# Kernel optimization log

Measured on AMD Instinct MI355X. Metric: run time of the kernel, lower is better.

The kernel has to match this reference:

```python
import jax, jax.numpy as jnp
import numpy as np

N_HEADS = 4
D_K = 64


def setup_inputs() -> dict:
    key = jax.random.key(0)
    k1, k2, k3, k4, k5 = jax.random.split(key, 5)
    C = 256
    return {
        "x": jax.random.normal(k1, (16, C, 32, 32), dtype=jnp.float32),
        "W_qkv": jax.random.normal(k2, (C, N_HEADS * D_K * 3), dtype=jnp.float32) * (C ** -0.5),
        "b_qkv": jax.random.normal(k3, (N_HEADS * D_K * 3,), dtype=jnp.float32) * 0.02,
        "W_out": jax.random.normal(k4, (N_HEADS * D_K, C), dtype=jnp.float32) * ((N_HEADS * D_K) ** -0.5),
        "b_out": jax.random.normal(k5, (C,), dtype=jnp.float32) * 0.02,
    }


def reference(x, W_qkv, b_qkv, W_out, b_out):
    # NOTE: the original forward never applies self.norm and ignores t.
    B, C, H, W = x.shape
    N = H * W
    scale = D_K ** -0.5
    xf = x.reshape(B, C, N).transpose(0, 2, 1)            # [B, N, C]
    qkv = (xf @ W_qkv + b_qkv).reshape(B, N, N_HEADS, 3 * D_K)
    q, k, v = jnp.split(qkv, 3, axis=-1)                  # each [B, N, H, dk]
    attn = jnp.einsum('bihd,bjhd->bijh', q, k) * scale    # [B, N, N, H]
    attn = jax.nn.softmax(attn, axis=2)                   # softmax over keys (j)
    res = jnp.einsum('bijh,bjhd->bihd', attn, v)          # [B, N, H, dk]
    res = res.reshape(B, N, N_HEADS * D_K)
    res = res @ W_out + b_out + xf                        # residual on flattened x
    return res.transpose(0, 2, 1).reshape(B, C, H, W)
```

## Files before the change

kernel.cpp:

```cpp
#include <hip/hip_runtime.h>
#include <math.h>

#define NN 1024

typedef __attribute__((ext_vector_type(8))) __bf16 bf16x8;
typedef __attribute__((ext_vector_type(4))) __bf16 bf16x4;
typedef __attribute__((ext_vector_type(4))) float f32x4;

__device__ __forceinline__ unsigned short f2bf(float f) {
    __bf16 h = (__bf16)f;
    return *(unsigned short*)&h;
}
__device__ __forceinline__ ushort4 pack4(float a, float b, float c, float d) {
    bf16x4 v;
    v[0] = (__bf16)a; v[1] = (__bf16)b; v[2] = (__bf16)c; v[3] = (__bf16)d;
    return *(ushort4*)&v;
}
__device__ __forceinline__ float bf2f(unsigned short u) {
    unsigned v = (unsigned)u << 16;
    return __uint_as_float(v);
}

__device__ __forceinline__ void async_cp16(const unsigned short* g, unsigned short* l) {
    __builtin_amdgcn_global_load_lds(
        (const __attribute__((address_space(1))) unsigned int*)g,
        (__attribute__((address_space(3))) unsigned int*)l,
        16, 0, 0);
}

__global__ __launch_bounds__(256) void prep_transpose(
    const float* __restrict__ x, const float* __restrict__ Wq,
    const float* __restrict__ Wo,
    unsigned short* __restrict__ xb, unsigned short* __restrict__ Wqt,
    unsigned short* __restrict__ Wot)
{
    __shared__ __align__(16) unsigned short T[64 * 72];
    const int bx = blockIdx.x;
    const int rt = blockIdx.y;
    const float* src; unsigned short* dst; int ncol, c0;
    if (bx < 256) {
        int b = bx >> 4; int ct = bx & 15;
        src = x + (size_t)b * 256 * 1024; dst = xb + (size_t)b * 1024 * 256;
        ncol = 1024; c0 = ct * 64;
    } else if (bx < 268) {
        src = Wq; dst = Wqt; ncol = 768; c0 = (bx - 256) * 64;
    } else {
        src = Wo; dst = Wot; ncol = 256; c0 = (bx - 268) * 64;
    }
    const int t = threadIdx.x;
    #pragma unroll
    for (int i = 0; i < 4; ++i) {
        int r  = i * 16 + (t >> 4);
        int c4 = (t & 15) * 4;
        float4 v = *(const float4*)&src[(size_t)(rt * 64 + r) * ncol + c0 + c4];
        *(ushort4*)&T[r * 72 + c4] = pack4(v.x, v.y, v.z, v.w);
    }
    __syncthreads();
    #pragma unroll
    for (int i = 0; i < 2; ++i) {
        int task = t + 256 * i;
        int c = task & 63, rs = task >> 6;
        ushort u8[8];
        #pragma unroll
        for (int k = 0; k < 8; ++k) u8[k] = T[(rs * 8 + k) * 72 + c];
        *(uint4*)&dst[(size_t)(c0 + c) * 256 + rt * 64 + rs * 8] = *(uint4*)u8;
    }
}

__global__ __launch_bounds__(256, 2) void qkv_gemm(
    const unsigned short* __restrict__ xb, const unsigned short* __restrict__ Wqt,
    const float* __restrict__ bias,
    unsigned short* __restrict__ Qb, unsigned short* __restrict__ Kb,
    unsigned short* __restrict__ Vtb)
{
    __shared__ __align__(16) unsigned short As[2][8192];
    __shared__ __align__(16) unsigned short Bs[2][8192];
    const int jt = blockIdx.x;
    const int m0 = blockIdx.y * 128;
    const int b  = m0 >> 10;
    const int n0 = m0 & 1023;
    const int t = threadIdx.x;
    const int w = t >> 6, lane = t & 63, quad = lane >> 4, cc = lane & 15;
    const int wm = (w & 1) * 64;
    const int wj = (w >> 1) * 64;

    f32x4 acc[4][4];
    #pragma unroll
    for (int ms = 0; ms < 4; ++ms)
        #pragma unroll
        for (int js = 0; js < 4; ++js) acc[ms][js] = (f32x4)(0.f);

    auto stage = [&](int k0, unsigned short* dA, unsigned short* dB) {
        #pragma unroll
        for (int i = 0; i < 4; ++i) {
            int f = i * 256 + t;
            int row = f >> 3;
            int gc  = (f & 7) ^ (row & 7);
            async_cp16(&xb[(size_t)(m0 + row) * 256 + k0 + gc * 8], &dA[f * 8]);
            async_cp16(&Wqt[(size_t)(jt * 128 + row) * 256 + k0 + gc * 8], &dB[f * 8]);
        }
    };

    stage(0, As[0], Bs[0]);
    __syncthreads();

    #pragma unroll
    for (int s = 0; s < 4; ++s) {
        const int cur = s & 1;
        if (s > 0) __syncthreads();
        if (s < 3) stage((s + 1) * 64, As[cur ^ 1], Bs[cur ^ 1]);

        #pragma unroll
        for (int ks = 0; ks < 2; ++ks) {
            bf16x8 af[4], bfr[4];
            #pragma unroll
            for (int ms = 0; ms < 4; ++ms) {
                int row = wm + ms * 16 + cc;
                int sc = (ks * 4 + quad) ^ (cc & 7);
                af[ms] = *(bf16x8*)&As[cur][row * 64 + sc * 8];
            }
            #pragma unroll
            for (int js = 0; js < 4; ++js) {
                int row = wj + js * 16 + cc;
                int sc = (ks * 4 + quad) ^ (cc & 7);
                bfr[js] = *(bf16x8*)&Bs[cur][row * 64 + sc * 8];
            }
            #pragma unroll
            for (int ms = 0; ms < 4; ++ms)
                #pragma unroll
                for (int js = 0; js < 4; ++js)
                    acc[ms][js] = __builtin_amdgcn_mfma_f32_16x16x32_bf16(
                        af[ms], bfr[js], acc[ms][js], 0, 0, 0);
        }
    }

    const int chunk = jt * 2 + (w >> 1);
    const int h = chunk / 3, type = chunk % 3;
    const size_t bh = (size_t)b * 4 + h;
    float bias_r[4];
    #pragma unroll
    for (int js = 0; js < 4; ++js) bias_r[js] = bias[jt * 128 + wj + js * 16 + cc];

    if (type == 2) {
        #pragma unroll
        for (int ms = 0; ms < 4; ++ms)
            #pragma unroll
            for (int js = 0; js < 4; ++js) {
                int dd = js * 16 + cc;
                int n = n0 + wm + ms * 16 + quad * 4;
                *(ushort4*)&Vtb[(bh * 64 + dd) * NN + n] =
                    pack4(acc[ms][js][0] + bias_r[js], acc[ms][js][1] + bias_r[js],
                          acc[ms][js][2] + bias_r[js], acc[ms][js][3] + bias_r[js]);
            }
    } else {
        unsigned short* dst = type ? Kb : Qb;
        const float sc = type ? 1.0f : 0.18033688011112042f;
        #pragma unroll
        for (int ms = 0; ms < 4; ++ms)
            #pragma unroll
            for (int js = 0; js < 4; ++js)
                #pragma unroll
                for (int r = 0; r < 4; ++r) {
                    int n = n0 + wm + ms * 16 + quad * 4 + r;
                    dst[(bh * NN + n) * 64 + js * 16 + cc] =
                        f2bf((acc[ms][js][r] + bias_r[js]) * sc);
                }
    }
}

__global__ __launch_bounds__(256, 4) void flash_attn(
    const unsigned short* __restrict__ Qb, const unsigned short* __restrict__ Kb,
    const unsigned short* __restrict__ Vtb, unsigned short* __restrict__ resb)
{
    __shared__ __align__(16) unsigned short QP[4096];
    __shared__ __align__(16) unsigned short Ks0[4096];
    __shared__ __align__(16) unsigned short Ks1[4096];
    __shared__ __align__(16) unsigned short Vt0[4096];
    __shared__ __align__(16) unsigned short Vt1[4096];

    const int blk = blockIdx.x;
    const int qt = blk & 15;
    const int h  = (blk >> 4) & 3;
    const int b  = blk >> 6;
    const int t  = threadIdx.x;
    const int w  = t >> 6;
    const int lane = t & 63;
    const int quad = lane >> 4;
    const int c    = lane & 15;

    const size_t bh = (size_t)(b * 4 + h);
    const unsigned short* Qg = Qb  + bh * NN * 64;
    const unsigned short* Kg = Kb  + bh * NN * 64;
    const unsigned short* Vg = Vtb + bh * 64 * NN;

    #pragma unroll
    for (int i = 0; i < 2; ++i) {
        int f = i * 256 + t;
        int row = f >> 3;
        int gc  = (f & 7) ^ (row & 7);
        async_cp16(&Qg[(size_t)(qt * 64 + row) * 64 + gc * 8], &QP[f * 8]);
        async_cp16(&Kg[(size_t)row * 64 + gc * 8], &Ks0[f * 8]);
        async_cp16(&Vg[(size_t)row * NN + gc * 8], &Vt0[f * 8]);
    }
    __syncthreads();

    bf16x8 qf[2];
    #pragma unroll
    for (int ks = 0; ks < 2; ++ks) {
        int sc_ = (ks * 4 + quad) ^ (c & 7);
        qf[ks] = *(bf16x8*)&QP[((w * 16 + c) * 8 + sc_) * 8];
    }

    float l_part = 0.f;
    f32x4 O[4];
    #pragma unroll
    for (int dt = 0; dt < 4; ++dt) O[dt] = (f32x4)(0.f);

    auto step = [&](int kt, const unsigned short* curK, const unsigned short* curV,
                    unsigned short* nxtK, unsigned short* nxtV,
                    bool pref, bool bar) {
        if (bar) __syncthreads();
        if (pref) {
            int ktn = kt + 1;
            #pragma unroll
            for (int i = 0; i < 2; ++i) {
                int f = i * 256 + t;
                int row = f >> 3;
                int gc  = (f & 7) ^ (row & 7);
                async_cp16(&Kg[(size_t)(ktn * 64 + row) * 64 + gc * 8], &nxtK[f * 8]);
                async_cp16(&Vg[(size_t)row * NN + ktn * 64 + gc * 8], &nxtV[f * 8]);
            }
        }

        f32x4 S[4];
        #pragma unroll
        for (int jt = 0; jt < 4; ++jt) S[jt] = (f32x4)(0.f);
        #pragma unroll
        for (int ks = 0; ks < 2; ++ks) {
            #pragma unroll
            for (int jt = 0; jt < 4; ++jt) {
                int sc_ = (ks * 4 + quad) ^ (c & 7);
                bf16x8 kf = *(bf16x8*)&curK[((jt * 16 + c) * 8 + sc_) * 8];
                S[jt] = __builtin_amdgcn_mfma_f32_16x16x32_bf16(kf, qf[ks], S[jt], 0, 0, 0);
            }
        }

        float p[4][4], rsj[4];
        #pragma unroll
        for (int jt = 0; jt < 4; ++jt) {
            #pragma unroll
            for (int r = 0; r < 4; ++r)
                p[jt][r] = __builtin_amdgcn_exp2f(S[jt][r]);
            rsj[jt] = (p[jt][0] + p[jt][1]) + (p[jt][2] + p[jt][3]);
        }
        l_part += (rsj[0] + rsj[1]) + (rsj[2] + rsj[3]);

        #pragma unroll
        for (int jt = 0; jt < 4; ++jt) {
            int scw = (jt * 2 + (quad >> 1)) ^ (c & 7);
            *(ushort4*)&QP[(w * 16 + c) * 64 + scw * 8 + (quad & 1) * 4] =
                pack4(p[jt][0], p[jt][1], p[jt][2], p[jt][3]);
        }

        #pragma unroll
        for (int js = 0; js < 2; ++js) {
            int scp = (js * 4 + quad) ^ (c & 7);
            bf16x8 pf = *(bf16x8*)&QP[(w * 16 + c) * 64 + scp * 8];
            #pragma unroll
            for (int dt = 0; dt < 4; ++dt) {
                int sc_ = (js * 4 + quad) ^ (c & 7);
                bf16x8 vf = *(bf16x8*)&curV[((dt * 16 + c) * 8 + sc_) * 8];
                O[dt] = __builtin_amdgcn_mfma_f32_16x16x32_bf16(pf, vf, O[dt], 0, 0, 0);
            }
        }
    };

    step(0, Ks0, Vt0, Ks1, Vt1, true, false);
    for (int kt2 = 0; kt2 < 7; ++kt2) {
        int kt = 2 * kt2 + 1;
        step(kt,     Ks1, Vt1, Ks0, Vt0, true, true);
        step(kt + 1, Ks0, Vt0, Ks1, Vt1, true, true);
    }
    step(15, Ks1, Vt1, Ks0, Vt0, false, true);

    float l_tot = l_part;
    l_tot += __shfl_xor(l_tot, 16);
    l_tot += __shfl_xor(l_tot, 32);

    float linv[4];
    #pragma unroll
    for (int r = 0; r < 4; ++r) linv[r] = 1.f / __shfl(l_tot, quad * 4 + r);
    #pragma unroll
    for (int dt = 0; dt < 4; ++dt)
        #pragma unroll
        for (int r = 0; r < 4; ++r) {
            int row = qt * 64 + w * 16 + quad * 4 + r;
            resb[((size_t)(b * NN + row)) * 256 + h * 64 + dt * 16 + c] =
                f2bf(O[dt][r] * linv[r]);
        }
}

__global__ __launch_bounds__(256, 4) void out_gemm(
    const unsigned short* __restrict__ resb, const unsigned short* __restrict__ Wot,
    const float* __restrict__ bias, const unsigned short* __restrict__ xb,
    float* __restrict__ out)
{
    __shared__ __align__(16) unsigned short As[2][4096];
    __shared__ __align__(16) unsigned short Bs[2][4096];
    const int n0 = blockIdx.x * 64;
    const int c0 = blockIdx.y * 64;
    const int b  = blockIdx.z;
    const int t = threadIdx.x;
    const int w = t >> 6, lane = t & 63, quad = lane >> 4, cc = lane & 15;
    const int wm = (w & 1) * 32;
    const int wj = (w >> 1) * 32;

    f32x4 acc[2][2];
    #pragma unroll
    for (int ms = 0; ms < 2; ++ms)
        #pragma unroll
        for (int js = 0; js < 2; ++js) acc[ms][js] = (f32x4)(0.f);

    auto stage = [&](int k0, unsigned short* dA, unsigned short* dB) {
        #pragma unroll
        for (int i = 0; i < 2; ++i) {
            int f = i * 256 + t;
            int row = f >> 3;
            int gc  = (f & 7) ^ (row & 7);
            async_cp16(&resb[((size_t)b * NN + n0 + row) * 256 + k0 + gc * 8], &dA[f * 8]);
            async_cp16(&Wot[(size_t)(c0 + row) * 256 + k0 + gc * 8], &dB[f * 8]);
        }
    };

    stage(0, As[0], Bs[0]);
    __syncthreads();

    #pragma unroll
    for (int s = 0; s < 4; ++s) {
        const int cur = s & 1;
        if (s > 0) __syncthreads();
        if (s < 3) stage((s + 1) * 64, As[cur ^ 1], Bs[cur ^ 1]);

        #pragma unroll
        for (int ks = 0; ks < 2; ++ks) {
            bf16x8 af[2], bfr[2];
            #pragma unroll
            for (int ms = 0; ms < 2; ++ms) {
                int row = wm + ms * 16 + cc;
                int sc = (ks * 4 + quad) ^ (cc & 7);
                af[ms] = *(bf16x8*)&As[cur][row * 64 + sc * 8];
            }
            #pragma unroll
            for (int js = 0; js < 2; ++js) {
                int row = wj + js * 16 + cc;
                int sc = (ks * 4 + quad) ^ (cc & 7);
                bfr[js] = *(bf16x8*)&Bs[cur][row * 64 + sc * 8];
            }
            #pragma unroll
            for (int ms = 0; ms < 2; ++ms)
                #pragma unroll
                for (int js = 0; js < 2; ++js)
                    acc[ms][js] = __builtin_amdgcn_mfma_f32_16x16x32_bf16(
                        af[ms], bfr[js], acc[ms][js], 0, 0, 0);
        }
    }

    #pragma unroll
    for (int js = 0; js < 2; ++js) {
        int cI = c0 + wj + js * 16 + cc;
        float bi = bias[cI];
        #pragma unroll
        for (int ms = 0; ms < 2; ++ms) {
            int n = n0 + wm + ms * 16 + quad * 4;
            size_t off = ((size_t)b * 256 + cI) * NN + n;
            float4 o;
            float* op = &o.x;
            #pragma unroll
            for (int r = 0; r < 4; ++r) {
                float xr = bf2f(xb[((size_t)b * NN + n + r) * 256 + cI]);
                op[r] = acc[ms][js][r] + bi + xr;
            }
            *(float4*)&out[off] = o;
        }
    }
}

extern "C" void kernel_launch(void* const* d_in, const int* in_sizes, int n_in,
                              void* d_out, int out_size, void* d_ws, size_t ws_size,
                              hipStream_t stream)
{
    const float* x     = (const float*)d_in[0];
    const float* W_qkv = (const float*)d_in[1];
    const float* b_qkv = (const float*)d_in[2];
    const float* W_out = (const float*)d_in[3];
    const float* b_out = (const float*)d_in[4];
    float* out = (float*)d_out;

    char* wsc = (char*)d_ws;
    unsigned short* xb   = (unsigned short*)(wsc);
    unsigned short* Wqt  = (unsigned short*)(wsc + ((size_t)8 << 20));
    unsigned short* Wot  = (unsigned short*)(wsc + ((size_t)8 << 20) + ((size_t)512 << 10));
    unsigned short* Qb   = (unsigned short*)(wsc + ((size_t)9  << 20));
    unsigned short* Kb   = (unsigned short*)(wsc + ((size_t)17 << 20));
    unsigned short* Vtb  = (unsigned short*)(wsc + ((size_t)25 << 20));
    unsigned short* resb = (unsigned short*)(wsc + ((size_t)33 << 20));

    prep_transpose<<<dim3(272, 4), 256, 0, stream>>>(x, W_qkv, W_out, xb, Wqt, Wot);
    qkv_gemm<<<dim3(6, 128), 256, 0, stream>>>(xb, Wqt, b_qkv, Qb, Kb, Vtb);
    flash_attn<<<dim3(1024), 256, 0, stream>>>(Qb, Kb, Vtb, resb);
    out_gemm<<<dim3(16, 4, 16), 256, 0, stream>>>(resb, Wot, b_out, xb, out);
}
```

Measured before the change: 131.3 us.

## Keep softmax probabilities in registers and feed PV via 16x16x16 MFMA

Drops the LDS round-trip for the P tile. The exp2 results now stay in registers and go straight into 16x16x16 bf16 MFMAs, whose operand layout matches the S accumulator layout, and V fragments are read at 4-element granularity. Q is loaded directly from global memory into registers instead of being staged through shared memory, which frees the QP buffer. The cost is twice as many MFMA instructions of half the K depth and more, narrower LDS reads of V. In exchange the LDS writes/reads of P disappear and shared memory use shrinks.

Result: no change. 131.0 us (-0.2%).

```diff
diff --git a/kernel.cpp b/kernel.cpp
--- a/kernel.cpp
+++ b/kernel.cpp
@@ -5,6 +5,7 @@
 
 typedef __attribute__((ext_vector_type(8))) __bf16 bf16x8;
 typedef __attribute__((ext_vector_type(4))) __bf16 bf16x4;
+typedef __attribute__((ext_vector_type(4))) short s16x4;
 typedef __attribute__((ext_vector_type(4))) float f32x4;
 
 __device__ __forceinline__ unsigned short f2bf(float f) {
@@ -19,6 +20,16 @@
 __device__ __forceinline__ float bf2f(unsigned short u) {
     unsigned v = (unsigned)u << 16;
     return __uint_as_float(v);
+}
+
+__device__ __forceinline__ f32x4 mfma16x16x16(ushort4 a, ushort4 b, f32x4 c) {
+#if __has_builtin(__builtin_amdgcn_mfma_f32_16x16x16_bf16)
+    return __builtin_amdgcn_mfma_f32_16x16x16_bf16(
+        *(bf16x4*)&a, *(bf16x4*)&b, c, 0, 0, 0);
+#else
+    return __builtin_amdgcn_mfma_f32_16x16x16bf16_1k(
+        *(s16x4*)&a, *(s16x4*)&b, c, 0, 0, 0);
+#endif
 }
 
 __device__ __forceinline__ void async_cp16(const unsigned short* g, unsigned short* l) {
@@ -172,7 +183,6 @@
     const unsigned short* __restrict__ Qb, const unsigned short* __restrict__ Kb,
     const unsigned short* __restrict__ Vtb, unsigned short* __restrict__ resb)
 {
-    __shared__ __align__(16) unsigned short QP[4096];
     __shared__ __align__(16) unsigned short Ks0[4096];
     __shared__ __align__(16) unsigned short Ks1[4096];
     __shared__ __align__(16) unsigned short Vt0[4096];
@@ -198,18 +208,15 @@
         int f = i * 256 + t;
         int row = f >> 3;
         int gc  = (f & 7) ^ (row & 7);
-        async_cp16(&Qg[(size_t)(qt * 64 + row) * 64 + gc * 8], &QP[f * 8]);
         async_cp16(&Kg[(size_t)row * 64 + gc * 8], &Ks0[f * 8]);
         async_cp16(&Vg[(size_t)row * NN + gc * 8], &Vt0[f * 8]);
     }
+    bf16x8 qf[2];
+    #pragma unroll
+    for (int ks = 0; ks < 2; ++ks)
+        qf[ks] = *(const bf16x8*)&Qg[(size_t)(qt * 64 + w * 16 + c) * 64 +
+                                     ks * 32 + quad * 8];
     __syncthreads();
-
-    bf16x8 qf[2];
-    #pragma unroll
-    for (int ks = 0; ks < 2; ++ks) {
-        int sc_ = (ks * 4 + quad) ^ (c & 7);
-        qf[ks] = *(bf16x8*)&QP[((w * 16 + c) * 8 + sc_) * 8];
-    }
 
     float l_part = 0.f;
     f32x4 O[4];
@@ -245,32 +252,25 @@
             }
         }
 
-        float p[4][4], rsj[4];
+        ushort4 Pf[4];
         #pragma unroll
         for (int jt = 0; jt < 4; ++jt) {
-            #pragma unroll
-            for (int r = 0; r < 4; ++r)
-                p[jt][r] = __builtin_amdgcn_exp2f(S[jt][r]);
-            rsj[jt] = (p[jt][0] + p[jt][1]) + (p[jt][2] + p[jt][3]);
-        }
-        l_part += (rsj[0] + rsj[1]) + (rsj[2] + rsj[3]);
+            float p0 = __builtin_amdgcn_exp2f(S[jt][0]);
+            float p1 = __builtin_amdgcn_exp2f(S[jt][1]);
+            float p2 = __builtin_amdgcn_exp2f(S[jt][2]);
+            float p3 = __builtin_amdgcn_exp2f(S[jt][3]);
+            l_part += (p0 + p1) + (p2 + p3);
+            Pf[jt] = pack4(p0, p1, p2, p3);
+        }
 
         #pragma unroll
         for (int jt = 0; jt < 4; ++jt) {
-            int scw = (jt * 2 + (quad >> 1)) ^ (c & 7);
-            *(ushort4*)&QP[(w * 16 + c) * 64 + scw * 8 + (quad & 1) * 4] =
-                pack4(p[jt][0], p[jt][1], p[jt][2], p[jt][3]);
-        }
-
-        #pragma unroll
-        for (int js = 0; js < 2; ++js) {
-            int scp = (js * 4 + quad) ^ (c & 7);
-            bf16x8 pf = *(bf16x8*)&QP[(w * 16 + c) * 64 + scp * 8];
             #pragma unroll
             for (int dt = 0; dt < 4; ++dt) {
-                int sc_ = (js * 4 + quad) ^ (c & 7);
-                bf16x8 vf = *(bf16x8*)&curV[((dt * 16 + c) * 8 + sc_) * 8];
-                O[dt] = __builtin_amdgcn_mfma_f32_16x16x32_bf16(pf, vf, O[dt], 0, 0, 0);
+                int sc_ = (jt * 2 + (quad >> 1)) ^ (c & 7);
+                ushort4 vfrag = *(ushort4*)&curV[(dt * 16 + c) * 64 +
+                                                 sc_ * 8 + (quad & 1) * 4];
+                O[dt] = mfma16x16x16(Pf[jt], vfrag, O[dt]);
             }
         }
     };
```
